# Optimization experiments

Measured on AMD Instinct MI355X. Metric: run time of the kernel, lower is better.

Reference implementation:

```python
import jax, jax.numpy as jnp
import numpy as np

N = 50000      # nodes
E = 800000     # edges (avg degree 16)
DIN = 128      # node_in_channels
DE = 16        # edge_in_channels
C1 = 64        # gat1_out_channels
H1 = 1         # num_heads
C2 = 64        # gat2_out_channels
HID = 256      # Edge_hidden_dim
NEG = 0.2      # negative_slope
DCLS = 2 * C2 + DE  # edge classifier input dim = 144


def _glorot(k, shape):
    fan = sum(shape)
    return jax.random.normal(k, shape, jnp.float32) * np.float32(np.sqrt(2.0 / fan))


def setup_inputs():
    key = jax.random.key(0)
    ks = jax.random.split(key, 30)
    inp = {
        'x': jax.random.normal(ks[0], (N, DIN), jnp.float32),
        'edge_attr': jax.random.normal(ks[1], (E, DE), jnp.float32),
        # GATv2Conv layer 1
        'W1l': _glorot(ks[2], (DIN, H1 * C1)), 'b1l': jnp.zeros((H1 * C1,), jnp.float32),
        'W1r': _glorot(ks[3], (DIN, H1 * C1)), 'b1r': jnp.zeros((H1 * C1,), jnp.float32),
        'We1': _glorot(ks[4], (DE, H1 * C1)),
        'att1': _glorot(ks[5], (H1, C1)),
        'bias1': jnp.zeros((H1 * C1,), jnp.float32),
        # GATv2Conv layer 2 (heads=1, concat=False)
        'W2l': _glorot(ks[6], (H1 * C1, C2)), 'b2l': jnp.zeros((C2,), jnp.float32),
        'W2r': _glorot(ks[7], (H1 * C1, C2)), 'b2r': jnp.zeros((C2,), jnp.float32),
        'We2': _glorot(ks[8], (DE, C2)),
        'att2': _glorot(ks[9], (1, C2)),
        'bias2': jnp.zeros((C2,), jnp.float32),
        # EdgeAttentionClassifier
        'Aw1': _glorot(ks[10], (DCLS, 64)), 'Ab1': jnp.zeros((64,), jnp.float32),
        'Aw2': _glorot(ks[11], (64, 1)), 'Ab2': jnp.zeros((1,), jnp.float32),
        'Cw1': _glorot(ks[12], (DCLS, HID)), 'Cb1': jnp.zeros((HID,), jnp.float32),
        'Cw2': _glorot(ks[13], (HID, 1)), 'Cb2': jnp.zeros((1,), jnp.float32),
        'edge_index': jax.random.randint(ks[14], (2, E), 0, N, dtype=jnp.int32),
    }
    return inp


def _gatv2_layer(x, src, dst, eattr, Wl, bl, Wr, br, We, att, bias, heads, out_ch, concat):
    n = x.shape[0]
    xl = (x @ Wl + bl).reshape(n, heads, out_ch)  # source transform
    xr = (x @ Wr + br).reshape(n, heads, out_ch)  # target transform
    e = (eattr @ We).reshape(-1, heads, out_ch)
    m = xl[src] + xr[dst] + e                      # [E, H, C]
    a = jnp.einsum('ehc,hc->eh', jax.nn.leaky_relu(m, NEG), att)
    # scatter-softmax over incoming edges of each destination node
    amax = jax.ops.segment_max(a, dst, num_segments=n)
    amax = jnp.where(jnp.isfinite(amax), amax, 0.0)
    ex = jnp.exp(a - amax[dst])
    den = jax.ops.segment_sum(ex, dst, num_segments=n)
    alpha = ex / den[dst]                          # [E, H]
    out = jax.ops.segment_sum(xl[src] * alpha[:, :, None], dst, num_segments=n)
    out = out.reshape(n, heads * out_ch) if concat else out.mean(axis=1)
    return out + bias


def reference(x, edge_attr, W1l, b1l, W1r, b1r, We1, att1, bias1,
              W2l, b2l, W2r, b2r, We2, att2, bias2,
              Aw1, Ab1, Aw2, Ab2, Cw1, Cb1, Cw2, Cb2, edge_index):
    src, dst = edge_index[0], edge_index[1]
    n = x.shape[0]
    # add self loops; self-loop edge_attr = mean of incoming edge attrs (PyG fill_value='mean')
    deg = jax.ops.segment_sum(jnp.ones(src.shape, x.dtype), dst, num_segments=n)
    loop_attr = jax.ops.segment_sum(edge_attr, dst, num_segments=n) / jnp.maximum(deg, 1.0)[:, None]
    ar = jnp.arange(n, dtype=src.dtype)
    src_sl = jnp.concatenate([src, ar])
    dst_sl = jnp.concatenate([dst, ar])
    ea_sl = jnp.concatenate([edge_attr, loop_attr], axis=0)

    h = jax.nn.elu(_gatv2_layer(x, src_sl, dst_sl, ea_sl, W1l, b1l, W1r, b1r, We1, att1, bias1, H1, C1, True))
    h2 = _gatv2_layer(h, src_sl, dst_sl, ea_sl, W2l, b2l, W2r, b2r, We2, att2, bias2, 1, C2, False)

    # edge classifier on ORIGINAL edges
    ef = jnp.concatenate([h2[src], h2[dst], edge_attr], axis=-1)  # [E, 144]
    aw = jax.nn.softmax(jax.nn.relu(ef @ Aw1 + Ab1) @ Aw2 + Ab2, axis=-1)  # [E,1] -> all ones
    wf = ef * aw
    out = (jax.nn.elu(wf @ Cw1 + Cb1) @ Cw2 + Cb2).squeeze(-1)
    return out
```

## Files before the change

### kernel.cpp

```cpp
#include <hip/hip_runtime.h>
#include <math.h>

#define NN   50000
#define NE   800000
#define ESL  (NE + NN)
#define DIN1 128
#define DE   16
#define C    64
#define HID  256
#define DCLS 144
#define KP   160
#define LDA  168
#define NEGS 0.2f
#define NPB  8
#define NBLK ((NN + 255) / 256)

typedef __attribute__((ext_vector_type(8))) short  short8;
typedef __attribute__((ext_vector_type(4))) float  f32x4;

__device__ __forceinline__ ushort f2bf(float f) {
    unsigned u = __float_as_uint(f);
    u += 0x7fffu + ((u >> 16) & 1u);
    return (ushort)(u >> 16);
}
__device__ __forceinline__ float bf2f(ushort u) {
    return __uint_as_float(((unsigned)u) << 16);
}
__device__ __forceinline__ float bflo(unsigned w) { return __uint_as_float(w << 16); }
__device__ __forceinline__ float bfhi(unsigned w) { return __uint_as_float(w & 0xffff0000u); }

__global__ void k_deg(const int* __restrict__ dst, int* __restrict__ deg) {
    int e = blockIdx.x * blockDim.x + threadIdx.x;
    if (e < NE) atomicAdd(&deg[dst[e]], 1);
}

__global__ void k_scan1(const int* __restrict__ deg, int* __restrict__ rowptr,
                        int* __restrict__ bsum) {
    __shared__ int s[256];
    int t = threadIdx.x;
    int i = blockIdx.x * 256 + t;
    int v = (i < NN) ? (deg[i] + 1) : 0;
    s[t] = v;
    __syncthreads();
    for (int off = 1; off < 256; off <<= 1) {
        int u = (t >= off) ? s[t - off] : 0;
        __syncthreads();
        s[t] += u;
        __syncthreads();
    }
    if (i < NN) rowptr[i] = s[t] - v;
    if (t == 255) bsum[blockIdx.x] = s[255];
}

__global__ void k_scan2(int* __restrict__ bsum, int* __restrict__ boff) {
    __shared__ int s[256];
    int t = threadIdx.x;
    int v = (t < NBLK) ? bsum[t] : 0;
    s[t] = v;
    __syncthreads();
    for (int off = 1; off < 256; off <<= 1) {
        int u = (t >= off) ? s[t - off] : 0;
        __syncthreads();
        s[t] += u;
        __syncthreads();
    }
    if (t < NBLK) boff[t] = s[t] - v;
}

__global__ void k_scan3(int* __restrict__ rowptr, const int* __restrict__ boff) {
    int i = blockIdx.x * 256 + threadIdx.x;
    if (i < NN) rowptr[i] += boff[blockIdx.x];
    if (i == 0) rowptr[NN] = ESL;
}

__global__ void k_scatter(const int* __restrict__ src, const int* __restrict__ dst,
                          const float* __restrict__ eattr,
                          const int* __restrict__ rowptr, int* __restrict__ cursor,
                          int* __restrict__ src_perm, ushort* __restrict__ eap) {
    int e = blockIdx.x * blockDim.x + threadIdx.x;
    if (e >= NE) return;
    int d = dst[e];
    int pos = atomicAdd(&cursor[d], 1);
    int idx = rowptr[d] + pos;
    src_perm[idx] = src[e];
    const float4* p4 = (const float4*)&eattr[(size_t)e * DE];
    float4 c0 = p4[0], c1 = p4[1], c2 = p4[2], c3 = p4[3];
    short8 r0, r1;
    r0[0]=f2bf(c0.x); r0[1]=f2bf(c0.y); r0[2]=f2bf(c0.z); r0[3]=f2bf(c0.w);
    r0[4]=f2bf(c1.x); r0[5]=f2bf(c1.y); r0[6]=f2bf(c1.z); r0[7]=f2bf(c1.w);
    r1[0]=f2bf(c2.x); r1[1]=f2bf(c2.y); r1[2]=f2bf(c2.z); r1[3]=f2bf(c2.w);
    r1[4]=f2bf(c3.x); r1[5]=f2bf(c3.y); r1[6]=f2bf(c3.z); r1[7]=f2bf(c3.w);
    short8* q = (short8*)&eap[(size_t)idx * DE];
    q[0] = r0; q[1] = r1;
}

__global__ void k_loop_csr(const int* __restrict__ rowptr,
                           ushort* __restrict__ eap, int* __restrict__ src_perm) {
    int wave = threadIdx.x >> 6, lane = threadIdx.x & 63;
    int d = blockIdx.x * 4 + wave;
    if (d >= NN) return;
    int j = lane & 15, g = lane >> 4;
    int kb = rowptr[d], ke1 = rowptr[d + 1] - 1;
    float sum = 0.f;
    for (int k = kb + g; k < ke1; k += 4)
        sum += bf2f(eap[(size_t)k * DE + j]);
    sum += __shfl_xor(sum, 16);
    sum += __shfl_xor(sum, 32);
    if (lane < 16)
        eap[(size_t)ke1 * DE + lane] = f2bf(sum / fmaxf((float)(ke1 - kb), 1.0f));
    if (lane == 16) src_perm[ke1] = d;
}

template<int DINT>
__global__ void k_lin(const float* __restrict__ x,
                      const float* __restrict__ Wl, const float* __restrict__ bl,
                      const float* __restrict__ Wr, const float* __restrict__ br,
                      ushort* __restrict__ xlb, float* __restrict__ xr) {
    int i0 = blockIdx.x * NPB;
    int t = threadIdx.x;
    int c = t & (C - 1);
    const float* W = (t < C) ? Wl : Wr;
    float bb = (t < C) ? bl[c] : br[c];
    float acc[NPB];
#pragma unroll
    for (int n = 0; n < NPB; ++n) acc[n] = bb;
    for (int k = 0; k < DINT; ++k) {
        float wk = W[k * C + c];
#pragma unroll
        for (int n = 0; n < NPB; ++n)
            acc[n] = fmaf(x[(i0 + n) * DINT + k], wk, acc[n]);
    }
    if (t < C) {
#pragma unroll
        for (int n = 0; n < NPB; ++n)
            xlb[(size_t)(i0 + n) * C + c] = f2bf(acc[n]);
    } else {
#pragma unroll
        for (int n = 0; n < NPB; ++n)
            xr[(size_t)(i0 + n) * C + c] = acc[n];
    }
}

template<int DO_ELU, int OUT_BF16>
__global__ __launch_bounds__(64, 4) void k_gat(
        const int* __restrict__ src_perm, const int* __restrict__ rowptr,
        const ushort* __restrict__ eap,
        const ushort* __restrict__ xlb, const float* __restrict__ xr,
        const float* __restrict__ We, const float* __restrict__ att,
        const float* __restrict__ bias, void* __restrict__ o_) {
    int d = blockIdx.x;
    int lane = threadIdx.x;
    int g = lane >> 4, l = lane & 15;
    int c0 = l * 4;
    float wreg[DE][4];
#pragma unroll
    for (int j = 0; j < DE; ++j) {
        float4 wv = *(const float4*)&We[j * C + c0];
        wreg[j][0] = wv.x; wreg[j][1] = wv.y; wreg[j][2] = wv.z; wreg[j][3] = wv.w;
    }
    float4 av4 = *(const float4*)&att[c0];
    float attv[4] = {av4.x, av4.y, av4.z, av4.w};
    float4 xr4 = *(const float4*)&xr[(size_t)d * C + c0];
    float xrv[4] = {xr4.x, xr4.y, xr4.z, xr4.w};

    float l_run = 0.f, n_run[4] = {0.f, 0.f, 0.f, 0.f};
    int kb = rowptr[d], ke = rowptr[d + 1];
    for (int k = kb; k < ke; k += 4) {
        int kk = k + g;
        bool valid = kk < ke;
        int kidx = valid ? kk : (ke - 1);
        int s = src_perm[kidx];
        uint2 xlr = *(const uint2*)&xlb[(size_t)s * C + c0];
        float xlv[4] = {bflo(xlr.x), bfhi(xlr.x), bflo(xlr.y), bfhi(xlr.y)};
        const uint4* ep = (const uint4*)&eap[(size_t)kidx * DE];
        uint4 e0 = ep[0], e1 = ep[1];
        float m[4];
#pragma unroll
        for (int i = 0; i < 4; ++i) m[i] = xlv[i] + xrv[i];
        unsigned ew[8] = {e0.x, e0.y, e0.z, e0.w, e1.x, e1.y, e1.z, e1.w};
#pragma unroll
        for (int wji = 0; wji < 8; ++wji) {
            float elo = bflo(ew[wji]), ehi = bfhi(ew[wji]);
#pragma unroll
            for (int i = 0; i < 4; ++i) {
                m[i] = fmaf(elo, wreg[2 * wji][i], m[i]);
                m[i] = fmaf(ehi, wreg[2 * wji + 1][i], m[i]);
            }
        }
        float p = 0.f;
#pragma unroll
        for (int i = 0; i < 4; ++i) {
            float t = fmaxf(m[i], NEGS * m[i]);
            p = fmaf(t, attv[i], p);
        }
        p += __shfl_xor(p, 1);
        p += __shfl_xor(p, 2);
        p += __shfl_xor(p, 4);
        p += __shfl_xor(p, 8);
        float pe = valid ? __expf(p) : 0.f;
        l_run += pe;
#pragma unroll
        for (int i = 0; i < 4; ++i) n_run[i] = fmaf(pe, xlv[i], n_run[i]);
    }
    l_run += __shfl_xor(l_run, 16);
    l_run += __shfl_xor(l_run, 32);
#pragma unroll
    for (int i = 0; i < 4; ++i) {
        n_run[i] += __shfl_xor(n_run[i], 16);
        n_run[i] += __shfl_xor(n_run[i], 32);
    }
    if (g == 0) {
        float4 bv = *(const float4*)&bias[c0];
        float bvv[4] = {bv.x, bv.y, bv.z, bv.w};
        float res[4];
#pragma unroll
        for (int i = 0; i < 4; ++i) {
            float v = n_run[i] / l_run + bvv[i];
            if (DO_ELU) v = (v > 0.f) ? v : (__expf(v) - 1.0f);
            res[i] = v;
        }
        if (OUT_BF16) {
            uint2 pk;
            pk.x = (unsigned)f2bf(res[0]) | ((unsigned)f2bf(res[1]) << 16);
            pk.y = (unsigned)f2bf(res[2]) | ((unsigned)f2bf(res[3]) << 16);
            *(uint2*)&((ushort*)o_)[(size_t)d * C + c0] = pk;
        } else {
            float4 pk = {res[0], res[1], res[2], res[3]};
            *(float4*)&((float*)o_)[(size_t)d * C + c0] = pk;
        }
    }
}

__global__ void k_cvt_w(const float* __restrict__ Cw1, short* __restrict__ Cw1T) {
    int n = blockIdx.x;
    int k = threadIdx.x;
    Cw1T[n * KP + k] = (k < DCLS) ? (short)f2bf(Cw1[k * HID + n]) : (short)0;
}

__global__ __launch_bounds__(256, 4) void k_cls_mfma(
        const int* __restrict__ src, const int* __restrict__ dst,
        const float* __restrict__ eattr, const short* __restrict__ h2b,
        const short* __restrict__ Cw1T, const float* __restrict__ Cb1,
        const float* __restrict__ Cw2, const float* __restrict__ Cb2,
        float* __restrict__ out) {
    __shared__ short sEF[64 * LDA];
    __shared__ float sOutW[4][64];
    int t = threadIdx.x;
    int ebase = blockIdx.x * 64;
    {
        int el = t & 63, part = t >> 6;
        int e = ebase + el;
        short8* q = (short8*)&sEF[el * LDA];
        if (part == 0) {
            const short8* p = (const short8*)&h2b[(size_t)src[e] * C];
#pragma unroll
            for (int i = 0; i < 8; ++i) q[i] = p[i];
        } else if (part == 1) {
            const short8* p = (const short8*)&h2b[(size_t)dst[e] * C];
#pragma unroll
            for (int i = 0; i < 8; ++i) q[8 + i] = p[i];
        } else if (part == 2) {
            const float4* p4 = (const float4*)&eattr[(size_t)e * DE];
            float4 c0 = p4[0], c1 = p4[1], c2 = p4[2], c3 = p4[3];
            short8 r0, r1;
            r0[0]=f2bf(c0.x); r0[1]=f2bf(c0.y); r0[2]=f2bf(c0.z); r0[3]=f2bf(c0.w);
            r0[4]=f2bf(c1.x); r0[5]=f2bf(c1.y); r0[6]=f2bf(c1.z); r0[7]=f2bf(c1.w);
            r1[0]=f2bf(c2.x); r1[1]=f2bf(c2.y); r1[2]=f2bf(c2.z); r1[3]=f2bf(c2.w);
            r1[4]=f2bf(c3.x); r1[5]=f2bf(c3.y); r1[6]=f2bf(c3.z); r1[7]=f2bf(c3.w);
            q[16] = r0; q[17] = r1;
        } else {
            short8 z = {0,0,0,0,0,0,0,0};
            q[18] = z; q[19] = z;
        }
    }
    __syncthreads();

    int lane = t & 63, wave = t >> 6;
    int l15 = lane & 15, quad = lane >> 4;
    int hb = wave * 64;

    float cb1v[4][4], cw2v[4][4];
#pragma unroll
    for (int mt = 0; mt < 4; ++mt) {
        float4 bv = *(const float4*)&Cb1[hb + mt * 16 + quad * 4];
        float4 wv = *(const float4*)&Cw2[hb + mt * 16 + quad * 4];
        cb1v[mt][0] = bv.x; cb1v[mt][1] = bv.y; cb1v[mt][2] = bv.z; cb1v[mt][3] = bv.w;
        cw2v[mt][0] = wv.x; cw2v[mt][1] = wv.y; cw2v[mt][2] = wv.z; cw2v[mt][3] = wv.w;
    }

    f32x4 acc[4][4];
#pragma unroll
    for (int mt = 0; mt < 4; ++mt) {
        f32x4 bi = {cb1v[mt][0], cb1v[mt][1], cb1v[mt][2], cb1v[mt][3]};
#pragma unroll
        for (int nt = 0; nt < 4; ++nt) acc[mt][nt] = bi;
    }

    const short8* Ap = (const short8*)Cw1T;
#pragma unroll
    for (int kk = 0; kk < 5; ++kk) {
        short8 a[4], b[4];
#pragma unroll
        for (int mt = 0; mt < 4; ++mt)
            a[mt] = Ap[(hb + mt * 16 + l15) * 20 + kk * 4 + quad];
#pragma unroll
        for (int nt = 0; nt < 4; ++nt)
            b[nt] = *(const short8*)&sEF[(nt * 16 + l15) * LDA + kk * 32 + quad * 8];
#pragma unroll
        for (int mt = 0; mt < 4; ++mt)
#pragma unroll
            for (int nt = 0; nt < 4; ++nt)
                acc[mt][nt] = __builtin_amdgcn_mfma_f32_16x16x32_bf16(
                    a[mt], b[nt], acc[mt][nt], 0, 0, 0);
    }

    float p[4] = {0.f, 0.f, 0.f, 0.f};
#pragma unroll
    for (int nt = 0; nt < 4; ++nt)
#pragma unroll
        for (int mt = 0; mt < 4; ++mt)
#pragma unroll
            for (int r = 0; r < 4; ++r) {
                float h = acc[mt][nt][r];
                float act = (h > 0.f) ? h : (__expf(h) - 1.0f);
                p[nt] = fmaf(act, cw2v[mt][r], p[nt]);
            }
#pragma unroll
    for (int nt = 0; nt < 4; ++nt) {
        p[nt] += __shfl_xor(p[nt], 16);
        p[nt] += __shfl_xor(p[nt], 32);
    }
    if (quad == 0) {
#pragma unroll
        for (int nt = 0; nt < 4; ++nt)
            sOutW[wave][nt * 16 + l15] = p[nt];
    }
    __syncthreads();
    if (t < 64)
        out[ebase + t] = sOutW[0][t] + sOutW[1][t] + sOutW[2][t] + sOutW[3][t] + Cb2[0];
}

extern "C" void kernel_launch(void* const* d_in, const int* in_sizes, int n_in,
                              void* d_out, int out_size, void* d_ws, size_t ws_size,
                              hipStream_t stream) {
    const float* x     = (const float*)d_in[0];
    const float* eattr = (const float*)d_in[1];
    const float* W1l   = (const float*)d_in[2];
    const float* b1l   = (const float*)d_in[3];
    const float* W1r   = (const float*)d_in[4];
    const float* b1r   = (const float*)d_in[5];
    const float* We1   = (const float*)d_in[6];
    const float* att1  = (const float*)d_in[7];
    const float* bias1 = (const float*)d_in[8];
    const float* W2l   = (const float*)d_in[9];
    const float* b2l   = (const float*)d_in[10];
    const float* W2r   = (const float*)d_in[11];
    const float* b2r   = (const float*)d_in[12];
    const float* We2   = (const float*)d_in[13];
    const float* att2  = (const float*)d_in[14];
    const float* bias2 = (const float*)d_in[15];
    const float* Cw1   = (const float*)d_in[20];
    const float* Cb1   = (const float*)d_in[21];
    const float* Cw2   = (const float*)d_in[22];
    const float* Cb2   = (const float*)d_in[23];
    const int*   eidx  = (const int*)d_in[24];
    const int* src = eidx;
    const int* dst = eidx + NE;
    float* out = (float*)d_out;

    int*    deg      = (int*)d_ws;
    int*    cursor   = deg + NN;
    int*    rowptr   = cursor + NN;
    int*    bsum     = rowptr + NN + 4;
    int*    boff     = bsum + 256;
    int*    src_perm = boff + 256;
    ushort* eap      = (ushort*)(src_perm + ESL);
    ushort* xlb      = eap + (size_t)ESL * DE;
    float*  xr       = (float*)(xlb + (size_t)NN * C);
    float*  o1       = xr + (size_t)64 * NN;
    short*  h2b      = (short*)(o1 + (size_t)64 * NN);
    short*  cw1t     = h2b + (size_t)NN * C;

    hipMemsetAsync(deg, 0, (size_t)(2 * NN) * sizeof(int), stream);

    k_deg<<<(NE + 255) / 256, 256, 0, stream>>>(dst, deg);
    k_scan1<<<NBLK, 256, 0, stream>>>(deg, rowptr, bsum);
    k_scan2<<<1, 256, 0, stream>>>(bsum, boff);
    k_scan3<<<NBLK, 256, 0, stream>>>(rowptr, boff);
    k_scatter<<<(NE + 255) / 256, 256, 0, stream>>>(src, dst, eattr, rowptr, cursor,
                                                    src_perm, eap);
    k_loop_csr<<<(NN + 3) / 4, 256, 0, stream>>>(rowptr, eap, src_perm);

    k_cvt_w<<<HID, KP, 0, stream>>>(Cw1, cw1t);

    k_lin<DIN1><<<NN / NPB, 128, 0, stream>>>(x, W1l, b1l, W1r, b1r, xlb, xr);
    k_gat<1, 0><<<NN, 64, 0, stream>>>(src_perm, rowptr, eap, xlb, xr,
                                       We1, att1, bias1, o1);

    k_lin<C><<<NN / NPB, 128, 0, stream>>>(o1, W2l, b2l, W2r, b2r, xlb, xr);
    k_gat<0, 1><<<NN, 64, 0, stream>>>(src_perm, rowptr, eap, xlb, xr,
                                       We2, att2, bias2, h2b);

    k_cls_mfma<<<NE / 64, 256, 0, stream>>>(src, dst, eattr, h2b, cw1t, Cb1, Cw2, Cb2, out);
}
```

Measured before the change: 732.0 us.

## Software-pipeline edge classifier with double-buffered LDS tiles across five tiles per block

Each classifier block now processes five 64-edge tiles and double-buffers the gathered edge features in LDS. The gather for the next tile is issued into registers while the MFMA work for the current tile runs, which is meant to hide gather latency. The LDS layout changes to a column-chunked format, and the zero-padded K tail is masked in registers. Launch bounds drop to three blocks per SM and the grid is five times smaller, so fewer blocks are available to hide latency and per-block register pressure rises.

```diff
diff --git a/kernel.cpp b/kernel.cpp
--- a/kernel.cpp
+++ b/kernel.cpp
@@ -10,10 +10,15 @@
 #define HID  256
 #define DCLS 144
 #define KP   160
-#define LDA  168
 #define NEGS 0.2f
 #define NPB  8
 #define NBLK ((NN + 255) / 256)
+
+#define TPB  5
+#define NBC  (NE / (TPB * 64))
+#define CH   1024
+#define BUFB (18 * CH)
+#define LDS_CLS (2 * BUFB + 2048)
 
 typedef __attribute__((ext_vector_type(8))) short  short8;
 typedef __attribute__((ext_vector_type(4))) float  f32x4;
@@ -237,107 +242,161 @@
     Cw1T[n * KP + k] = (k < DCLS) ? (short)f2bf(Cw1[k * HID + n]) : (short)0;
 }
 
-__global__ __launch_bounds__(256, 4) void k_cls_mfma(
+
+__device__ __forceinline__ void cls_load(int ebase, int tid,
+        const int* __restrict__ src, const int* __restrict__ dst,
+        const short* __restrict__ h2b, const float* __restrict__ eattr,
+        uint4* f, float4* ea) {
+    int r = tid & 127, h = tid >> 7;
+    int node = (r < 64) ? src[ebase + r] : dst[ebase + r - 64];
+    const uint4* g = (const uint4*)(h2b + (size_t)node * C + h * 32);
+#pragma unroll
+    for (int i = 0; i < 4; ++i) f[i] = g[i];
+    *ea = *(const float4*)&eattr[(size_t)(ebase + (tid >> 2)) * DE + (tid & 3) * 4];
+}
+
+__device__ __forceinline__ void cls_write(char* __restrict__ buf, int tid,
+        const uint4* f, const float4* ea) {
+    int r = tid & 127, h = tid >> 7;
+    int el = r & 63;
+    int cb = ((r >> 6) << 3) + (h << 2);
+    char* p = buf + cb * CH + el * 16;
+#pragma unroll
+    for (int i = 0; i < 4; ++i) *(uint4*)(p + i * CH) = f[i];
+    uint2 pk;
+    pk.x = (unsigned)f2bf(ea->x) | ((unsigned)f2bf(ea->y) << 16);
+    pk.y = (unsigned)f2bf(ea->z) | ((unsigned)f2bf(ea->w) << 16);
+    int eg = tid >> 2, q = tid & 3;
+    *(uint2*)(buf + (16 + (q >> 1)) * CH + eg * 16 + (q & 1) * 8) = pk;
+}
+
+template<int BUF>
+__device__ __forceinline__ void cls_compute(const char* lds, int tid, int hb,
+        const char* ApB, const int* voffA, const int* vbB, int quad, int l15,
+        const float* __restrict__ Cb1, const float* __restrict__ Cw2,
+        float* so) {
+    f32x4 acc[4][4];
+#pragma unroll
+    for (int mt = 0; mt < 4; ++mt) {
+        float4 bv = *(const float4*)&Cb1[hb + mt * 16 + quad * 4];
+        f32x4 bi = {bv.x, bv.y, bv.z, bv.w};
+#pragma unroll
+        for (int nt = 0; nt < 4; ++nt) acc[mt][nt] = bi;
+    }
+#pragma unroll
+    for (int kk = 0; kk < 5; ++kk) {
+        short8 a[4], b[4];
+#pragma unroll
+        for (int mt = 0; mt < 4; ++mt)
+            a[mt] = *(const short8*)(ApB + voffA[mt] + kk * 64);
+        if (kk < 4) {
+#pragma unroll
+            for (int nt = 0; nt < 4; ++nt)
+                b[nt] = *(const short8*)(lds + BUF * BUFB + kk * 4096 + vbB[nt]);
+        } else {
+            short8 z = {0,0,0,0,0,0,0,0};
+#pragma unroll
+            for (int nt = 0; nt < 4; ++nt) {
+                short8 v = *(const short8*)(lds + BUF * BUFB + 16384 + vbB[nt]);
+                b[nt] = (quad < 2) ? v : z;
+            }
+        }
+#pragma unroll
+        for (int mt = 0; mt < 4; ++mt)
+#pragma unroll
+            for (int nt = 0; nt < 4; ++nt)
+                acc[mt][nt] = __builtin_amdgcn_mfma_f32_16x16x32_bf16(
+                    a[mt], b[nt], acc[mt][nt], 0, 0, 0);
+    }
+    float p[4] = {0.f, 0.f, 0.f, 0.f};
+#pragma unroll
+    for (int mt = 0; mt < 4; ++mt) {
+        float4 wv = *(const float4*)&Cw2[hb + mt * 16 + quad * 4];
+        float w[4] = {wv.x, wv.y, wv.z, wv.w};
+#pragma unroll
+        for (int nt = 0; nt < 4; ++nt)
+#pragma unroll
+            for (int r = 0; r < 4; ++r) {
+                float h = acc[mt][nt][r];
+                float act = (h > 0.f) ? h : (__expf(h) - 1.0f);
+                p[nt] = fmaf(act, w[r], p[nt]);
+            }
+    }
+#pragma unroll
+    for (int nt = 0; nt < 4; ++nt) {
+        p[nt] += __shfl_xor(p[nt], 16);
+        p[nt] += __shfl_xor(p[nt], 32);
+    }
+    if (quad == 0) {
+        int wave = tid >> 6;
+#pragma unroll
+        for (int nt = 0; nt < 4; ++nt)
+            so[BUF * 256 + wave * 64 + nt * 16 + l15] = p[nt];
+    }
+}
+
+__device__ __forceinline__ void cls_final(const float* so, int par, int ebase,
+                                          int tid, float cb2,
+                                          float* __restrict__ out) {
+    if (tid < 64)
+        out[ebase + tid] = so[par * 256 + tid] + so[par * 256 + 64 + tid]
+                         + so[par * 256 + 128 + tid] + so[par * 256 + 192 + tid]
+                         + cb2;
+}
+
+__global__ __launch_bounds__(256, 3) void k_cls_mfma(
         const int* __restrict__ src, const int* __restrict__ dst,
         const float* __restrict__ eattr, const short* __restrict__ h2b,
         const short* __restrict__ Cw1T, const float* __restrict__ Cb1,
         const float* __restrict__ Cw2, const float* __restrict__ Cb2,
         float* __restrict__ out) {
-    __shared__ short sEF[64 * LDA];
-    __shared__ float sOutW[4][64];
-    int t = threadIdx.x;
-    int ebase = blockIdx.x * 64;
-    {
-        int el = t & 63, part = t >> 6;
-        int e = ebase + el;
-        short8* q = (short8*)&sEF[el * LDA];
-        if (part == 0) {
-            const short8* p = (const short8*)&h2b[(size_t)src[e] * C];
-#pragma unroll
-            for (int i = 0; i < 8; ++i) q[i] = p[i];
-        } else if (part == 1) {
-            const short8* p = (const short8*)&h2b[(size_t)dst[e] * C];
-#pragma unroll
-            for (int i = 0; i < 8; ++i) q[8 + i] = p[i];
-        } else if (part == 2) {
-            const float4* p4 = (const float4*)&eattr[(size_t)e * DE];
-            float4 c0 = p4[0], c1 = p4[1], c2 = p4[2], c3 = p4[3];
-            short8 r0, r1;
-            r0[0]=f2bf(c0.x); r0[1]=f2bf(c0.y); r0[2]=f2bf(c0.z); r0[3]=f2bf(c0.w);
-            r0[4]=f2bf(c1.x); r0[5]=f2bf(c1.y); r0[6]=f2bf(c1.z); r0[7]=f2bf(c1.w);
-            r1[0]=f2bf(c2.x); r1[1]=f2bf(c2.y); r1[2]=f2bf(c2.z); r1[3]=f2bf(c2.w);
-            r1[4]=f2bf(c3.x); r1[5]=f2bf(c3.y); r1[6]=f2bf(c3.z); r1[7]=f2bf(c3.w);
-            q[16] = r0; q[17] = r1;
-        } else {
-            short8 z = {0,0,0,0,0,0,0,0};
-            q[18] = z; q[19] = z;
-        }
-    }
-    __syncthreads();
-
-    int lane = t & 63, wave = t >> 6;
+    __shared__ __align__(16) char lds[LDS_CLS];
+    int tid = threadIdx.x;
+    int lane = tid & 63, wave = tid >> 6;
     int l15 = lane & 15, quad = lane >> 4;
     int hb = wave * 64;
-
-    float cb1v[4][4], cw2v[4][4];
-#pragma unroll
-    for (int mt = 0; mt < 4; ++mt) {
-        float4 bv = *(const float4*)&Cb1[hb + mt * 16 + quad * 4];
-        float4 wv = *(const float4*)&Cw2[hb + mt * 16 + quad * 4];
-        cb1v[mt][0] = bv.x; cb1v[mt][1] = bv.y; cb1v[mt][2] = bv.z; cb1v[mt][3] = bv.w;
-        cw2v[mt][0] = wv.x; cw2v[mt][1] = wv.y; cw2v[mt][2] = wv.z; cw2v[mt][3] = wv.w;
-    }
-
-    f32x4 acc[4][4];
-#pragma unroll
-    for (int mt = 0; mt < 4; ++mt) {
-        f32x4 bi = {cb1v[mt][0], cb1v[mt][1], cb1v[mt][2], cb1v[mt][3]};
-#pragma unroll
-        for (int nt = 0; nt < 4; ++nt) acc[mt][nt] = bi;
-    }
-
-    const short8* Ap = (const short8*)Cw1T;
-#pragma unroll
-    for (int kk = 0; kk < 5; ++kk) {
-        short8 a[4], b[4];
-#pragma unroll
-        for (int mt = 0; mt < 4; ++mt)
-            a[mt] = Ap[(hb + mt * 16 + l15) * 20 + kk * 4 + quad];
-#pragma unroll
-        for (int nt = 0; nt < 4; ++nt)
-            b[nt] = *(const short8*)&sEF[(nt * 16 + l15) * LDA + kk * 32 + quad * 8];
-#pragma unroll
-        for (int mt = 0; mt < 4; ++mt)
-#pragma unroll
-            for (int nt = 0; nt < 4; ++nt)
-                acc[mt][nt] = __builtin_amdgcn_mfma_f32_16x16x32_bf16(
-                    a[mt], b[nt], acc[mt][nt], 0, 0, 0);
-    }
-
-    float p[4] = {0.f, 0.f, 0.f, 0.f};
+    int e0 = blockIdx.x * (TPB * 64);
+    const char* ApB = (const char*)Cw1T;
+    int voffA[4], vbB[4];
+#pragma unroll
+    for (int mt = 0; mt < 4; ++mt)
+        voffA[mt] = (hb + mt * 16 + l15) * (KP * 2) + quad * 16;
 #pragma unroll
     for (int nt = 0; nt < 4; ++nt)
-#pragma unroll
-        for (int mt = 0; mt < 4; ++mt)
-#pragma unroll
-            for (int r = 0; r < 4; ++r) {
-                float h = acc[mt][nt][r];
-                float act = (h > 0.f) ? h : (__expf(h) - 1.0f);
-                p[nt] = fmaf(act, cw2v[mt][r], p[nt]);
-            }
-#pragma unroll
-    for (int nt = 0; nt < 4; ++nt) {
-        p[nt] += __shfl_xor(p[nt], 16);
-        p[nt] += __shfl_xor(p[nt], 32);
-    }
-    if (quad == 0) {
-#pragma unroll
-        for (int nt = 0; nt < 4; ++nt)
-            sOutW[wave][nt * 16 + l15] = p[nt];
-    }
-    __syncthreads();
-    if (t < 64)
-        out[ebase + t] = sOutW[0][t] + sOutW[1][t] + sOutW[2][t] + sOutW[3][t] + Cb2[0];
+        vbB[nt] = quad * CH + (nt * 16 + l15) * 16;
+    float* so = (float*)(lds + 2 * BUFB);
+    float cb2 = Cb2[0];
+    char* buf0 = lds;
+    char* buf1 = lds + BUFB;
+
+    uint4 fA[4], fB[4];
+    float4 eaA, eaB;
+    cls_load(e0, tid, src, dst, h2b, eattr, fA, &eaA);
+    cls_write(buf0, tid, fA, &eaA);
+    cls_load(e0 + 64, tid, src, dst, h2b, eattr, fA, &eaA);
+    __syncthreads();
+    cls_compute<0>(lds, tid, hb, ApB, voffA, vbB, quad, l15, Cb1, Cw2, so);
+    cls_write(buf1, tid, fA, &eaA);
+    cls_load(e0 + 128, tid, src, dst, h2b, eattr, fB, &eaB);
+    __syncthreads();
+    cls_final(so, 0, e0, tid, cb2, out);
+    cls_compute<1>(lds, tid, hb, ApB, voffA, vbB, quad, l15, Cb1, Cw2, so);
+    cls_write(buf0, tid, fB, &eaB);
+    cls_load(e0 + 192, tid, src, dst, h2b, eattr, fA, &eaA);
+    __syncthreads();
+    cls_final(so, 1, e0 + 64, tid, cb2, out);
+    cls_compute<0>(lds, tid, hb, ApB, voffA, vbB, quad, l15, Cb1, Cw2, so);
+    cls_write(buf1, tid, fA, &eaA);
+    cls_load(e0 + 256, tid, src, dst, h2b, eattr, fB, &eaB);
+    __syncthreads();
+    cls_final(so, 0, e0 + 128, tid, cb2, out);
+    cls_compute<1>(lds, tid, hb, ApB, voffA, vbB, quad, l15, Cb1, Cw2, so);
+    cls_write(buf0, tid, fB, &eaB);
+    __syncthreads();
+    cls_final(so, 1, e0 + 192, tid, cb2, out);
+    cls_compute<0>(lds, tid, hb, ApB, voffA, vbB, quad, l15, Cb1, Cw2, so);
+    __syncthreads();
+    cls_final(so, 0, e0 + 256, tid, cb2, out);
 }
 
 extern "C" void kernel_launch(void* const* d_in, const int* in_sizes, int n_in,
@@ -401,5 +460,5 @@
     k_gat<0, 1><<<NN, 64, 0, stream>>>(src_perm, rowptr, eap, xlb, xr,
                                        We2, att2, bias2, h2b);
 
-    k_cls_mfma<<<NE / 64, 256, 0, stream>>>(src, dst, eattr, h2b, cw1t, Cb1, Cw2, Cb2, out);
-}
+    k_cls_mfma<<<NBC, 256, 0, stream>>>(src, dst, eattr, h2b, cw1t, Cb1, Cw2, Cb2, out);
+}
```

New measurement: 776.1 us. 6.0% more time.

## Restructure classifier LDS layout to chunk-major and split hidden dim into two passes

Applied to the files above, without the earlier changes.

The edge-classifier kernel now stores gathered edge features in LDS in a chunk-major layout (16-byte chunks indexed by k-group, edges contiguous), so MFMA B-operand reads are conflict-free without padding. The gather is spread over all 256 threads: each loads half a node row, and edge attributes are converted in parallel. The hidden dimension is processed in two passes of 32 rows per wave, cutting accumulator registers, and launch bounds rise to 5 blocks per CU for occupancy. In exchange, the epilogue reduces 8 partial sums instead of 4, and the zero K-padding is now handled in registers rather than stored in LDS.

```diff
diff --git a/kernel.cpp b/kernel.cpp
--- a/kernel.cpp
+++ b/kernel.cpp
@@ -10,10 +10,12 @@
 #define HID  256
 #define DCLS 144
 #define KP   160
-#define LDA  168
 #define NEGS 0.2f
 #define NPB  8
 #define NBLK ((NN + 255) / 256)
+
+#define CH   1024
+#define LDS_CLS (18 * CH + 2048)
 
 typedef __attribute__((ext_vector_type(8))) short  short8;
 typedef __attribute__((ext_vector_type(4))) float  f32x4;
@@ -237,107 +239,115 @@
     Cw1T[n * KP + k] = (k < DCLS) ? (short)f2bf(Cw1[k * HID + n]) : (short)0;
 }
 
-__global__ __launch_bounds__(256, 4) void k_cls_mfma(
+__global__ __launch_bounds__(256, 5) void k_cls_mfma(
         const int* __restrict__ src, const int* __restrict__ dst,
         const float* __restrict__ eattr, const short* __restrict__ h2b,
         const short* __restrict__ Cw1T, const float* __restrict__ Cb1,
         const float* __restrict__ Cw2, const float* __restrict__ Cb2,
         float* __restrict__ out) {
-    __shared__ short sEF[64 * LDA];
-    __shared__ float sOutW[4][64];
-    int t = threadIdx.x;
+    __shared__ __align__(16) char lds[LDS_CLS];
+    int tid = threadIdx.x;
     int ebase = blockIdx.x * 64;
+
     {
-        int el = t & 63, part = t >> 6;
-        int e = ebase + el;
-        short8* q = (short8*)&sEF[el * LDA];
-        if (part == 0) {
-            const short8* p = (const short8*)&h2b[(size_t)src[e] * C];
-#pragma unroll
-            for (int i = 0; i < 8; ++i) q[i] = p[i];
-        } else if (part == 1) {
-            const short8* p = (const short8*)&h2b[(size_t)dst[e] * C];
-#pragma unroll
-            for (int i = 0; i < 8; ++i) q[8 + i] = p[i];
-        } else if (part == 2) {
-            const float4* p4 = (const float4*)&eattr[(size_t)e * DE];
-            float4 c0 = p4[0], c1 = p4[1], c2 = p4[2], c3 = p4[3];
-            short8 r0, r1;
-            r0[0]=f2bf(c0.x); r0[1]=f2bf(c0.y); r0[2]=f2bf(c0.z); r0[3]=f2bf(c0.w);
-            r0[4]=f2bf(c1.x); r0[5]=f2bf(c1.y); r0[6]=f2bf(c1.z); r0[7]=f2bf(c1.w);
-            r1[0]=f2bf(c2.x); r1[1]=f2bf(c2.y); r1[2]=f2bf(c2.z); r1[3]=f2bf(c2.w);
-            r1[4]=f2bf(c3.x); r1[5]=f2bf(c3.y); r1[6]=f2bf(c3.z); r1[7]=f2bf(c3.w);
-            q[16] = r0; q[17] = r1;
-        } else {
-            short8 z = {0,0,0,0,0,0,0,0};
-            q[18] = z; q[19] = z;
-        }
+        int r = tid & 127, h = tid >> 7;
+        int el = r & 63;
+        int node = (r < 64) ? src[ebase + el] : dst[ebase + el];
+        const uint4* g = (const uint4*)(h2b + (size_t)node * C + h * 32);
+        uint4 f0 = g[0], f1 = g[1], f2 = g[2], f3 = g[3];
+        int cb = ((r >> 6) << 3) + (h << 2);
+        char* p = lds + cb * CH + el * 16;
+        *(uint4*)(p) = f0;
+        *(uint4*)(p + CH) = f1;
+        *(uint4*)(p + 2 * CH) = f2;
+        *(uint4*)(p + 3 * CH) = f3;
+        int eg = tid >> 2, q = tid & 3;
+        float4 ea = *(const float4*)&eattr[(size_t)(ebase + eg) * DE + q * 4];
+        uint2 pk;
+        pk.x = (unsigned)f2bf(ea.x) | ((unsigned)f2bf(ea.y) << 16);
+        pk.y = (unsigned)f2bf(ea.z) | ((unsigned)f2bf(ea.w) << 16);
+        *(uint2*)(lds + (16 + (q >> 1)) * CH + eg * 16 + (q & 1) * 8) = pk;
     }
     __syncthreads();
 
-    int lane = t & 63, wave = t >> 6;
+    int lane = tid & 63, wave = tid >> 6;
     int l15 = lane & 15, quad = lane >> 4;
-    int hb = wave * 64;
-
-    float cb1v[4][4], cw2v[4][4];
-#pragma unroll
-    for (int mt = 0; mt < 4; ++mt) {
-        float4 bv = *(const float4*)&Cb1[hb + mt * 16 + quad * 4];
-        float4 wv = *(const float4*)&Cw2[hb + mt * 16 + quad * 4];
-        cb1v[mt][0] = bv.x; cb1v[mt][1] = bv.y; cb1v[mt][2] = bv.z; cb1v[mt][3] = bv.w;
-        cw2v[mt][0] = wv.x; cw2v[mt][1] = wv.y; cw2v[mt][2] = wv.z; cw2v[mt][3] = wv.w;
-    }
-
-    f32x4 acc[4][4];
-#pragma unroll
-    for (int mt = 0; mt < 4; ++mt) {
-        f32x4 bi = {cb1v[mt][0], cb1v[mt][1], cb1v[mt][2], cb1v[mt][3]};
-#pragma unroll
-        for (int nt = 0; nt < 4; ++nt) acc[mt][nt] = bi;
-    }
-
-    const short8* Ap = (const short8*)Cw1T;
-#pragma unroll
-    for (int kk = 0; kk < 5; ++kk) {
-        short8 a[4], b[4];
-#pragma unroll
-        for (int mt = 0; mt < 4; ++mt)
-            a[mt] = Ap[(hb + mt * 16 + l15) * 20 + kk * 4 + quad];
-#pragma unroll
-        for (int nt = 0; nt < 4; ++nt)
-            b[nt] = *(const short8*)&sEF[(nt * 16 + l15) * LDA + kk * 32 + quad * 8];
-#pragma unroll
-        for (int mt = 0; mt < 4; ++mt)
+    float* so = (float*)(lds + 18 * CH);
+    const char* ApB = (const char*)Cw1T;
+    int vbB[4];
+#pragma unroll
+    for (int nt = 0; nt < 4; ++nt)
+        vbB[nt] = quad * CH + (nt * 16 + l15) * 16;
+
+#pragma unroll
+    for (int ps = 0; ps < 2; ++ps) {
+        int hb = ps * 128 + wave * 32;
+        f32x4 acc[2][4];
+#pragma unroll
+        for (int mt = 0; mt < 2; ++mt) {
+            float4 bv = *(const float4*)&Cb1[hb + mt * 16 + quad * 4];
+            f32x4 bi = {bv.x, bv.y, bv.z, bv.w};
+#pragma unroll
+            for (int nt = 0; nt < 4; ++nt) acc[mt][nt] = bi;
+        }
+#pragma unroll
+        for (int kk = 0; kk < 5; ++kk) {
+            short8 a[2], b[4];
+#pragma unroll
+            for (int mt = 0; mt < 2; ++mt)
+                a[mt] = *(const short8*)(ApB
+                          + (hb + mt * 16 + l15) * (KP * 2) + quad * 16 + kk * 64);
+            if (kk < 4) {
+#pragma unroll
+                for (int nt = 0; nt < 4; ++nt)
+                    b[nt] = *(const short8*)(lds + kk * 4096 + vbB[nt]);
+            } else {
+                short8 z = {0,0,0,0,0,0,0,0};
+#pragma unroll
+                for (int nt = 0; nt < 4; ++nt) {
+                    short8 v = *(const short8*)(lds + 16 * CH + vbB[nt]);
+                    b[nt] = (quad < 2) ? v : z;
+                }
+            }
+#pragma unroll
+            for (int mt = 0; mt < 2; ++mt)
+#pragma unroll
+                for (int nt = 0; nt < 4; ++nt)
+                    acc[mt][nt] = __builtin_amdgcn_mfma_f32_16x16x32_bf16(
+                        a[mt], b[nt], acc[mt][nt], 0, 0, 0);
+        }
+        float p[4] = {0.f, 0.f, 0.f, 0.f};
+#pragma unroll
+        for (int mt = 0; mt < 2; ++mt) {
+            float4 wv = *(const float4*)&Cw2[hb + mt * 16 + quad * 4];
+            float w[4] = {wv.x, wv.y, wv.z, wv.w};
 #pragma unroll
             for (int nt = 0; nt < 4; ++nt)
-                acc[mt][nt] = __builtin_amdgcn_mfma_f32_16x16x32_bf16(
-                    a[mt], b[nt], acc[mt][nt], 0, 0, 0);
-    }
-
-    float p[4] = {0.f, 0.f, 0.f, 0.f};
-#pragma unroll
-    for (int nt = 0; nt < 4; ++nt)
-#pragma unroll
-        for (int mt = 0; mt < 4; ++mt)
-#pragma unroll
-            for (int r = 0; r < 4; ++r) {
-                float h = acc[mt][nt][r];
-                float act = (h > 0.f) ? h : (__expf(h) - 1.0f);
-                p[nt] = fmaf(act, cw2v[mt][r], p[nt]);
-            }
-#pragma unroll
-    for (int nt = 0; nt < 4; ++nt) {
-        p[nt] += __shfl_xor(p[nt], 16);
-        p[nt] += __shfl_xor(p[nt], 32);
-    }
-    if (quad == 0) {
-#pragma unroll
-        for (int nt = 0; nt < 4; ++nt)
-            sOutW[wave][nt * 16 + l15] = p[nt];
+#pragma unroll
+                for (int r = 0; r < 4; ++r) {
+                    float hv = acc[mt][nt][r];
+                    float act = (hv > 0.f) ? hv : (__expf(hv) - 1.0f);
+                    p[nt] = fmaf(act, w[r], p[nt]);
+                }
+        }
+#pragma unroll
+        for (int nt = 0; nt < 4; ++nt) {
+            p[nt] += __shfl_xor(p[nt], 16);
+            p[nt] += __shfl_xor(p[nt], 32);
+        }
+        if (quad == 0) {
+#pragma unroll
+            for (int nt = 0; nt < 4; ++nt)
+                so[ps * 256 + wave * 64 + nt * 16 + l15] = p[nt];
+        }
     }
     __syncthreads();
-    if (t < 64)
-        out[ebase + t] = sOutW[0][t] + sOutW[1][t] + sOutW[2][t] + sOutW[3][t] + Cb2[0];
+    if (tid < 64) {
+        float s = Cb2[0];
+#pragma unroll
+        for (int i = 0; i < 8; ++i) s += so[i * 64 + tid];
+        out[ebase + tid] = s;
+    }
 }
 
 extern "C" void kernel_launch(void* const* d_in, const int* in_sizes, int n_in,
```

Result: no change. 719.0 us (-1.8%).
